# Kernel optimization log

Measured on AMD Instinct MI355X. Metric: run time of the kernel, lower is better.

Reference implementation:

```python
import jax, jax.numpy as jnp
import numpy as np

V = 50257   # vocab size (output_size / num_words)
H = 500     # hidden_size
S = 256     # source sequence length
MAXLEN = 64 # greedy decode steps
SOS = 1


def _gru_scan(xs, Wih, Whh, bih, bhh, reverse=False):
    """Run a GRU over xs: (S, Din) -> (outputs (S,H), final hidden (H,)).
    PyTorch gate order: r, z, n."""
    gx = xs @ Wih.T + bih  # (S, 3H), input-side gates precomputed
    Hh = Whh.shape[1]
    h0 = jnp.zeros((Hh,), dtype=xs.dtype)

    def step(h, g):
        gh = Whh @ h + bhh
        rx, zx, nx = jnp.split(g, 3)
        rh, zh, nh = jnp.split(gh, 3)
        r = jax.nn.sigmoid(rx + rh)
        z = jax.nn.sigmoid(zx + zh)
        n = jnp.tanh(nx + r * nh)
        h2 = (1.0 - z) * n + z * h
        return h2, h2

    hT, ys = jax.lax.scan(step, h0, gx, reverse=reverse)
    return ys, hT


def _gru_cell(x, h, Wih, Whh, bih, bhh):
    gx = Wih @ x + bih
    gh = Whh @ h + bhh
    rx, zx, nx = jnp.split(gx, 3)
    rh, zh, nh = jnp.split(gh, 3)
    r = jax.nn.sigmoid(rx + rh)
    z = jax.nn.sigmoid(zx + zh)
    n = jnp.tanh(nx + r * nh)
    return (1.0 - z) * n + z * h


def setup_inputs() -> dict:
    key = jax.random.key(0)
    ks = jax.random.split(key, 32)

    def p(k, shape):
        return jax.random.normal(k, shape, dtype=jnp.float32) * 0.05

    inp = {}
    inp["input_seq"] = jax.random.randint(ks[0], (S, 1), 0, V)
    inp["input_length"] = S
    inp["max_length"] = MAXLEN
    inp["emb"] = p(ks[1], (V, H))
    i = 2
    for name, din in [("enc0f", H), ("enc0b", H), ("enc1f", 2 * H), ("enc1b", 2 * H)]:
        inp[name + "_Wih"] = p(ks[i], (3 * H, din)); i += 1
        inp[name + "_Whh"] = p(ks[i], (3 * H, H)); i += 1
        inp[name + "_bih"] = p(ks[i], (3 * H,)); i += 1
        inp[name + "_bhh"] = p(ks[i], (3 * H,)); i += 1
    inp["dec_Wih"] = p(ks[i], (2, 3 * H, H)); i += 1
    inp["dec_Whh"] = p(ks[i], (2, 3 * H, H)); i += 1
    inp["dec_bih"] = p(ks[i], (2, 3 * H)); i += 1
    inp["dec_bhh"] = p(ks[i], (2, 3 * H)); i += 1
    inp["concat_W"] = p(ks[i], (H, 2 * H)); i += 1
    inp["concat_b"] = p(ks[i], (H,)); i += 1
    inp["out_W"] = p(ks[i], (V, H)); i += 1
    inp["out_b"] = p(ks[i], (V,)); i += 1
    return inp


def reference(input_seq, input_length, max_length, emb,
              enc0f_Wih, enc0f_Whh, enc0f_bih, enc0f_bhh,
              enc0b_Wih, enc0b_Whh, enc0b_bih, enc0b_bhh,
              enc1f_Wih, enc1f_Whh, enc1f_bih, enc1f_bhh,
              enc1b_Wih, enc1b_Whh, enc1b_bih, enc1b_bhh,
              dec_Wih, dec_Whh, dec_bih, dec_bhh,
              concat_W, concat_b, out_W, out_b):
    tokens = input_seq[:, 0]  # batch = 1
    ex = emb[tokens]          # (S, H) embedding lookup (dropout is eval no-op)

    # --- bidirectional 2-layer encoder GRU (full-length seq, batch=1) ---
    y0f, h0f = _gru_scan(ex, enc0f_Wih, enc0f_Whh, enc0f_bih, enc0f_bhh)
    y0b, h0b = _gru_scan(ex, enc0b_Wih, enc0b_Whh, enc0b_bih, enc0b_bhh, reverse=True)
    x1 = jnp.concatenate([y0f, y0b], axis=1)  # (S, 2H)
    y1f, _ = _gru_scan(x1, enc1f_Wih, enc1f_Whh, enc1f_bih, enc1f_bhh)
    y1b, _ = _gru_scan(x1, enc1b_Wih, enc1b_Whh, enc1b_bih, enc1b_bhh, reverse=True)
    enc_out = y1f + y1b  # (S, H): outputs[:, :H] + outputs[:, H:]

    # encoder_hidden[:n_layers] = [layer0_fwd, layer0_bwd] (PyTorch ordering)
    h_dec0 = jnp.stack([h0f, h0b])  # (2, H)

    def step(carry, _):
        h, tok = carry
        x = emb[tok]  # (H,)
        hs = []
        for l in range(2):  # 2 decoder GRU layers (dropout off in eval)
            hl = _gru_cell(x, h[l], dec_Wih[l], dec_Whh[l], dec_bih[l], dec_bhh[l])
            hs.append(hl)
            x = hl
        h2 = jnp.stack(hs)
        rnn = x  # (H,) top-layer output
        scores = enc_out @ rnn                 # dot attention: (S,)
        w = jax.nn.softmax(scores)
        ctx = w @ enc_out                      # (H,)
        c = jnp.tanh(concat_W @ jnp.concatenate([rnn, ctx]) + concat_b)
        probs = jax.nn.softmax(out_W @ c + out_b)  # (V,)
        tok2 = jnp.argmax(probs).astype(jnp.int32)
        return (h2, tok2), (tok2, probs)

    init = (h_dec0, jnp.asarray(SOS, dtype=jnp.int32))
    _, (all_tokens, all_probs) = jax.lax.scan(step, init, None, length=int(max_length))
    return all_tokens, all_probs
```

## Files before the change

kernel.cpp:

```cpp
#include <hip/hip_runtime.h>
#include <math.h>

typedef unsigned long long ull;

constexpr int H    = 500;
constexpr int H3   = 1500;
constexpr int SEQ  = 256;
constexpr int V    = 50257;
constexpr int TDEC = 64;
constexpr int NLT  = (V + 255) / 256;
constexpr int SB   = 50;
constexpr int UPB  = 10;
constexpr int NDB  = 512;
constexpr int VPB  = (V + NDB - 1) / NDB;
constexpr int WB   = 63;

__device__ __forceinline__ float sigmoidf_(float x) { return 1.f / (1.f + expf(-x)); }

__device__ __forceinline__ float wred(float v) {
  #pragma unroll
  for (int off = 32; off > 0; off >>= 1) v += __shfl_down(v, off, 64);
  return v;
}

__device__ __forceinline__ float gload(const float* p) {
  return __hip_atomic_load((float*)p, __ATOMIC_RELAXED, __HIP_MEMORY_SCOPE_AGENT);
}
__device__ __forceinline__ void gstore(float* p, float v) {
  __hip_atomic_store(p, v, __ATOMIC_RELAXED, __HIP_MEMORY_SCOPE_AGENT);
}
__device__ __forceinline__ int gload_i(const int* p) {
  return __hip_atomic_load((int*)p, __ATOMIC_RELAXED, __HIP_MEMORY_SCOPE_AGENT);
}
__device__ __forceinline__ ull gload64(const ull* p) {
  return __hip_atomic_load((ull*)p, __ATOMIC_RELAXED, __HIP_MEMORY_SCOPE_AGENT);
}
__device__ __forceinline__ void gstore64(ull* p, ull v) {
  __hip_atomic_store(p, v, __ATOMIC_RELAXED, __HIP_MEMORY_SCOPE_AGENT);
}

template<int N, int SLP>
__device__ __forceinline__ void poll_tags(const ull* tags, unsigned want,
                                          float* dst, int tid) {
  constexpr int NW = (N + 63) / 64;
  if (tid < 64) {
    ull v[NW];
    bool ok;
    do {
      ok = true;
      #pragma unroll
      for (int j = 0; j < NW; ++j) {
        int k = tid + (j << 6);
        if (k < N) {
          v[j] = gload64(&tags[k]);
          if ((unsigned)(v[j] >> 32) != want) ok = false;
        }
      }
      if (!ok) __builtin_amdgcn_s_sleep(SLP);
    } while (!ok);
    #pragma unroll
    for (int j = 0; j < NW; ++j) {
      int k = tid + (j << 6);
      if (k < N) dst[k] = __uint_as_float((unsigned)v[j]);
    }
  }
  __syncthreads();
}

__device__ __forceinline__ void poll2_tags(const ull* tA, float* dA,
                                           const ull* tB, float* dB,
                                           unsigned want, int tid) {
  if (tid < 64) {
    ull va[8], vb[4];
    bool ok;
    do {
      ok = true;
      #pragma unroll
      for (int j = 0; j < 8; ++j) {
        int k = tid + (j << 6);
        if (k < 500) {
          va[j] = gload64(&tA[k]);
          if ((unsigned)(va[j] >> 32) != want) ok = false;
        }
      }
      #pragma unroll
      for (int j = 0; j < 4; ++j) {
        int k = tid + (j << 6);
        vb[j] = gload64(&tB[k]);
        if ((unsigned)(vb[j] >> 32) != want) ok = false;
      }
      if (!ok) __builtin_amdgcn_s_sleep(1);
    } while (!ok);
    #pragma unroll
    for (int j = 0; j < 8; ++j) {
      int k = tid + (j << 6);
      if (k < 500) dA[k] = __uint_as_float((unsigned)va[j]);
    }
    #pragma unroll
    for (int j = 0; j < 4; ++j) {
      int k = tid + (j << 6);
      dB[k] = __uint_as_float((unsigned)vb[j]);
    }
  }
  __syncthreads();
}

__global__ void init_k(ull* ttok) {
  if (threadIdx.x == 0) ttok[0] = (1ull << 32) | 1ull;
}

__global__ void embed_k(const int* __restrict__ seq, const float* __restrict__ emb,
                        float* __restrict__ ex) {
  int t = blockIdx.x;
  int tok = seq[t];
  for (int i = threadIdx.x; i < H; i += blockDim.x)
    ex[(size_t)t * H + i] = emb[(size_t)tok * H + i];
}

__global__ __launch_bounds__(256) void gemm_nt(const float* __restrict__ X,
                                               const float* __restrict__ W,
                                               const float* __restrict__ bias,
                                               float* __restrict__ C,
                                               int M, int N, int K) {
  __shared__ float Xs[64][17];
  __shared__ float Ws[64][17];
  int bm = blockIdx.y * 64, bn = blockIdx.x * 64;
  int tid = threadIdx.x;
  int tx = tid % 16, ty = tid / 16;
  float acc[4][4] = {};
  for (int k0 = 0; k0 < K; k0 += 16) {
    for (int i = tid; i < 64 * 16; i += 256) {
      int m = i / 16, k = i % 16;
      int gm = bm + m, gk = k0 + k, gn = bn + m;
      Xs[m][k] = (gm < M && gk < K) ? X[(size_t)gm * K + gk] : 0.f;
      Ws[m][k] = (gn < N && gk < K) ? W[(size_t)gn * K + gk] : 0.f;
    }
    __syncthreads();
    #pragma unroll
    for (int k = 0; k < 16; ++k) {
      float xv[4], wv[4];
      #pragma unroll
      for (int i = 0; i < 4; ++i) xv[i] = Xs[ty * 4 + i][k];
      #pragma unroll
      for (int j = 0; j < 4; ++j) wv[j] = Ws[tx * 4 + j][k];
      #pragma unroll
      for (int i = 0; i < 4; ++i)
        #pragma unroll
        for (int j = 0; j < 4; ++j) acc[i][j] += xv[i] * wv[j];
    }
    __syncthreads();
  }
  for (int i = 0; i < 4; ++i) {
    int gm = bm + ty * 4 + i;
    if (gm >= M) continue;
    for (int j = 0; j < 4; ++j) {
      int gn = bn + tx * 4 + j;
      if (gn >= N) continue;
      C[(size_t)gm * N + gn] = acc[i][j] + bias[gn];
    }
  }
}

__global__ __launch_bounds__(512, 1) void gru_scan_tag(
    const float* __restrict__ gxF, const float* __restrict__ gxB,
    const float* __restrict__ WhhF, const float* __restrict__ WhhB,
    const float* __restrict__ bhhF, const float* __restrict__ bhhB,
    ull* __restrict__ tAF, ull* __restrict__ tBF,
    ull* __restrict__ tAB, ull* __restrict__ tBB,
    float* __restrict__ yF, float* __restrict__ yB, int ystride) {
  __shared__ float gates[32];
  __shared__ float h_lds[512];
  int dir = blockIdx.x / SB;
  int bu  = blockIdx.x % SB;
  int u0  = bu * UPB;
  const float* gx  = dir ? gxB : gxF;
  const float* Whh = dir ? WhhB : WhhF;
  const float* bhh = dir ? bhhB : bhhF;
  ull* tagA = dir ? tAB : tAF;
  ull* tagB = dir ? tBB : tBF;
  float* y  = dir ? yB : yF;
  int tid = threadIdx.x, lane = tid & 63, wid = tid >> 6;

  float wreg[4][8];
  #pragma unroll
  for (int rr = 0; rr < 4; ++rr) {
    int r = wid + 8 * rr;
    #pragma unroll
    for (int j = 0; j < 8; ++j) {
      int k = lane + 64 * j;
      wreg[rr][j] = (r < 30 && k < 500)
          ? Whh[(size_t)((r / UPB) * 500 + u0 + (r % UPB)) * 500 + k] : 0.f;
    }
  }
  int u = u0 + tid;
  float br = 0.f, bz = 0.f, bn = 0.f;
  if (tid < UPB) { br = bhh[u]; bz = bhh[500 + u]; bn = bhh[1000 + u]; }
  h_lds[tid] = 0.f;
  __syncthreads();

  for (int t = 0; t < SEQ; ++t) {
    ull* wout = (t & 1) ? tagA : tagB;
    ull* win  = (t & 1) ? tagB : tagA;
    int teff = dir ? (SEQ - 1 - t) : t;

    float gxr = 0.f, gxz = 0.f, gxn = 0.f;
    if (tid < UPB) {
      const float* g = gx + (size_t)teff * H3;
      gxr = g[u]; gxz = g[500 + u]; gxn = g[1000 + u];
    }

    if (t > 0 && wid == 0) {
      ull v[8];
      for (;;) {
        bool ok = true;
        #pragma unroll
        for (int j = 0; j < 8; ++j) {
          int k = lane + 64 * j;
          if (k < 500) {
            v[j] = gload64(&win[k]);
            if ((unsigned)(v[j] >> 32) != (unsigned)t) ok = false;
          }
        }
        if (ok) break;
        __builtin_amdgcn_s_sleep(1);
      }
      #pragma unroll
      for (int j = 0; j < 8; ++j) {
        int k = lane + 64 * j;
        if (k < 500) h_lds[k] = __uint_as_float((unsigned)v[j]);
      }
    }
    __syncthreads();

    float hold = (tid < UPB) ? h_lds[u] : 0.f;
    float hreg[8];
    #pragma unroll
    for (int j = 0; j < 8; ++j) {
      int k = lane + 64 * j;
      hreg[j] = (k < 500) ? h_lds[k] : 0.f;
    }
    #pragma unroll
    for (int rr = 0; rr < 4; ++rr) {
      int r = wid + 8 * rr;
      if (r < 30) {
        float acc = 0.f;
        #pragma unroll
        for (int j = 0; j < 8; ++j) acc += wreg[rr][j] * hreg[j];
        acc = wred(acc);
        if (lane == 0) gates[r] = acc;
      }
    }
    __syncthreads();
    if (tid < UPB) {
      float rr = sigmoidf_(gxr + gates[tid]           + br);
      float zz = sigmoidf_(gxz + gates[UPB + tid]     + bz);
      float nn = tanhf(    gxn + rr * (gates[2 * UPB + tid] + bn));
      float hp = (1.f - zz) * nn + zz * hold;
      ull pv = ((ull)(unsigned)(t + 1) << 32) | (ull)__float_as_uint(hp);
      gstore64(&wout[u], pv);
      y[(size_t)teff * ystride + u] = hp;
    }
  }
}

__global__ void seed_k(const ull* __restrict__ tf, const ull* __restrict__ tb,
                       ull* __restrict__ th0a, ull* __restrict__ th1a) {
  int i = threadIdx.x;
  if (i < 500) {
    th0a[i] = (ull)(unsigned)tf[i];
    th1a[i] = (ull)(unsigned)tb[i];
  }
}

__global__ void add_k(const float* __restrict__ a, const float* __restrict__ b,
                      float* __restrict__ c, int n) {
  int i = blockIdx.x * blockDim.x + threadIdx.x;
  if (i < n) c[i] = a[i] + b[i];
}

__global__ __launch_bounds__(256) void transposeE_k(const float* __restrict__ A,
                                                    float* __restrict__ B) {
  __shared__ float t[64][65];
  int c0 = blockIdx.x * 64;
  int r0 = blockIdx.y * 64;
  int tx = threadIdx.x & 63, ty = threadIdx.x >> 6;
  #pragma unroll
  for (int i = 0; i < 64; i += 4) {
    int r = r0 + ty + i, c = c0 + tx;
    if (r < SEQ && c < 500) t[ty + i][tx] = A[(size_t)r * 500 + c];
  }
  __syncthreads();
  #pragma unroll
  for (int i = 0; i < 64; i += 4) {
    int c = c0 + ty + i, r = r0 + tx;
    if (c < 500 && r < SEQ) B[(size_t)c * SEQ + r] = t[tx][ty + i];
  }
}

__device__ __forceinline__ void cell_unit_tag(int u, int lane,
    const float* xf, const float* hf,
    const float* __restrict__ Wih, const float* __restrict__ Whh,
    const float* __restrict__ bih, const float* __restrict__ bhh,
    ull* htag, unsigned want) {
  float g[6];
  #pragma unroll
  for (int kind = 0; kind < 6; ++kind) {
    const float* row = (kind < 3) ? (Wih + (size_t)(kind * 500 + u) * 500)
                                  : (Whh + (size_t)((kind - 3) * 500 + u) * 500);
    const float* vec = (kind < 3) ? xf : hf;
    float acc = 0.f;
    #pragma unroll
    for (int j = 0; j < 8; ++j) {
      int k = lane + 64 * j;
      if (k < 500) acc += row[k] * vec[k];
    }
    g[kind] = wred(acc);
  }
  if (lane == 0) {
    float r = sigmoidf_(g[0] + bih[u]        + g[3] + bhh[u]);
    float z = sigmoidf_(g[1] + bih[500 + u]  + g[4] + bhh[500 + u]);
    float n = tanhf(    g[2] + bih[1000 + u] + r * (g[5] + bhh[1000 + u]));
    float hv = (1.f - z) * n + z * hf[u];
    gstore64(&htag[u], ((ull)want << 32) | (ull)__float_as_uint(hv));
  }
}

__global__ __launch_bounds__(512, 4) void dec_persist(
    const float* __restrict__ emb,
    const float* __restrict__ dWih, const float* __restrict__ dWhh,
    const float* __restrict__ dbih, const float* __restrict__ dbhh,
    const float* __restrict__ enc_out, const float* __restrict__ enc_outT,
    const float* __restrict__ cW, const float* __restrict__ cb,
    const float* __restrict__ outW, const float* __restrict__ outb,
    ull* __restrict__ th0a, ull* __restrict__ th0b,
    ull* __restrict__ th1a, ull* __restrict__ th1b,
    ull* __restrict__ tsc, ull* __restrict__ tctx, ull* __restrict__ tcvec,
    ull* __restrict__ ttok,
    float* __restrict__ lg0, float* __restrict__ lg1,
    float* __restrict__ pm, float* __restrict__ ps, int* __restrict__ pix,
    float* __restrict__ stats, float* __restrict__ out_tokens,
    float* __restrict__ out_probs, int* __restrict__ dcnt) {
  __shared__ float4 v4[250];
  __shared__ float hfull[512];
  __shared__ float red[256], sc[256];
  __shared__ float wm[8], wsum[8]; __shared__ int wix[8];
  __shared__ float mm[512], ms[512]; __shared__ int mi[512];
  __shared__ int lastf, sh_tk;
  float* xf = (float*)v4;
  float* hf = xf + 500;
  int tid = threadIdx.x, lane = tid & 63, wid = tid >> 6, blk = blockIdx.x;
  bool worker = blk < WB;
  int u = blk * 8 + wid;

  for (int st = 0; st < TDEC; ++st) {
    unsigned want = (unsigned)(st + 1);
    ull* h0r = (st & 1) ? th0b : th0a;
    ull* h0w = (st & 1) ? th0a : th0b;
    ull* h1r = (st & 1) ? th1b : th1a;
    ull* h1w = (st & 1) ? th1a : th1b;
    float* lg_w = (st & 1) ? lg1 : lg0;
    const float* lg_r = (st & 1) ? lg0 : lg1;

    if (worker) {
      if (tid == 0) {
        ull tv;
        for (;;) {
          tv = gload64(ttok);
          if ((unsigned)(tv >> 32) == want) break;
          __builtin_amdgcn_s_sleep(1);
        }
        sh_tk = (int)(unsigned)tv;
      }
      __syncthreads();
      int tk = sh_tk;
      if (tid >= 64) {
        for (int i = tid - 64; i < 500; i += 448) xf[i] = emb[(size_t)tk * 500 + i];
      } else {
        #pragma unroll
        for (int j = 0; j < 8; ++j) {
          int k = tid + (j << 6);
          if (k < 500) hf[k] = __uint_as_float((unsigned)gload64(&h0r[k]));
        }
      }
      __syncthreads();
      if (u < 500) cell_unit_tag(u, lane, xf, hf, dWih, dWhh, dbih, dbhh, h0w, want);
      __syncthreads();

      if (tid >= 64) {
        for (int i = tid - 64; i < 500; i += 448)
          hf[i] = __uint_as_float((unsigned)gload64(&h1r[i]));
      }
      poll_tags<500, 1>(h0w, want, xf, tid);
      if (u < 500) cell_unit_tag(u, lane, xf, hf,
          dWih + 750000, dWhh + 750000, dbih + 1500, dbhh + 1500, h1w, want);
      __syncthreads();

      if (blk < 32) {
        poll_tags<500, 1>(h1w, want, hfull, tid);
        int s = blk * 8 + wid;
        const float* row = enc_out + (size_t)s * 500;
        float acc = 0.f;
        #pragma unroll
        for (int j = 0; j < 8; ++j) {
          int k = lane + 64 * j;
          if (k < 500) acc += row[k] * hfull[k];
        }
        acc = wred(acc);
        if (lane == 0) gstore64(&tsc[s], ((ull)want << 32) | (ull)__float_as_uint(acc));
        poll_tags<256, 1>(tsc, want, sc, tid);
      } else {
        poll2_tags(h1w, hfull, tsc, sc, want, tid);
      }

      {
        float myv = (tid < 256) ? sc[tid] : 0.f;
        if (tid < 256) red[tid] = myv;
        __syncthreads();
        for (int s = 128; s > 0; s >>= 1) {
          if (tid < s) red[tid] = fmaxf(red[tid], red[tid + s]);
          __syncthreads();
        }
        float m = red[0]; __syncthreads();
        float e = 0.f;
        if (tid < 256) { e = expf(myv - m); red[tid] = e; }
        __syncthreads();
        for (int s = 128; s > 0; s >>= 1) {
          if (tid < s) red[tid] += red[tid + s];
          __syncthreads();
        }
        float inv = 1.f / red[0]; __syncthreads();
        if (tid < 256) sc[tid] = e * inv;
        __syncthreads();
        int j = blk * 8 + wid;
        if (j < 500) {
          const float* col = enc_outT + (size_t)j * SEQ;
          float acc = 0.f;
          #pragma unroll
          for (int q = 0; q < 4; ++q) {
            int s = lane + 64 * q;
            acc += sc[s] * col[s];
          }
          acc = wred(acc);
          if (lane == 0) gstore64(&tctx[j], ((ull)want << 32) | (ull)__float_as_uint(acc));
        }
      }

      if (tid >= 64) for (int i = tid - 64; i < 500; i += 448) xf[i] = hfull[i];
      poll_tags<500, 1>(tctx, want, hf, tid);
      {
        int i = blk * 8 + wid;
        if (i < 500) {
          const float* row = cW + (size_t)i * 1000;
          float acc = 0.f;
          #pragma unroll
          for (int j = 0; j < 16; ++j) {
            int k = lane + 64 * j;
            if (k < 1000) acc += row[k] * xf[k];
          }
          acc = wred(acc);
          if (lane == 0)
            gstore64(&tcvec[i], ((ull)want << 32) | (ull)__float_as_uint(tanhf(acc + cb[i])));
        }
      }
      __syncthreads();
    } else {
      if (tid == 0) {
        while ((unsigned)(gload64(ttok) >> 32) < want) __builtin_amdgcn_s_sleep(2);
      }
      __syncthreads();
      if (st > 0) {
        float mM = gload(&stats[2 * (st - 1)]), iS = gload(&stats[2 * (st - 1) + 1]);
        int base = blk * VPB;
        for (int r = tid; r < VPB; r += 512) {
          int v = base + r;
          if (v < V) out_probs[(size_t)(st - 1) * V + v] = expf(lg_r[v] - mM) * iS;
        }
      }
    }

    if (worker) poll_tags<500, 1>(tcvec, want, xf, tid);
    else        poll_tags<500, 4>(tcvec, want, xf, tid);
    const float4* c4 = v4;
    {
      int lstart = wid * 13, lend = lstart + 13;
      if (lstart > VPB) lstart = VPB;
      if (lend > VPB) lend = VPB;
      int r0 = blk * VPB + lstart, r1 = blk * VPB + lend; if (r1 > V) r1 = V;
      float m = -1e30f, ssum = 0.f; int ix = V;
      for (int rb = r0; rb < r1; rb += 8) {
        int nr = r1 - rb; if (nr > 8) nr = 8;
        float4 wv0[8], wv1[8];
        #pragma unroll
        for (int rr = 0; rr < 8; ++rr) {
          wv0[rr] = (lane < 125 && rr < nr)
              ? ((const float4*)(outW + (size_t)(rb + rr) * 500))[lane]
              : make_float4(0.f, 0.f, 0.f, 0.f);
        }
        #pragma unroll
        for (int rr = 0; rr < 8; ++rr) {
          int k4 = lane + 64;
          wv1[rr] = (k4 < 125 && rr < nr)
              ? ((const float4*)(outW + (size_t)(rb + rr) * 500))[k4]
              : make_float4(0.f, 0.f, 0.f, 0.f);
        }
        float a[8];
        #pragma unroll
        for (int rr = 0; rr < 8; ++rr) a[rr] = 0.f;
        if (lane < 125) {
          float4 cc = c4[lane];
          #pragma unroll
          for (int rr = 0; rr < 8; ++rr) {
            if (rr < nr) {
              float4 w4 = wv0[rr];
              a[rr] += w4.x * cc.x + w4.y * cc.y + w4.z * cc.z + w4.w * cc.w;
            }
          }
        }
        if (lane + 64 < 125) {
          float4 cc = c4[lane + 64];
          #pragma unroll
          for (int rr = 0; rr < 8; ++rr) {
            if (rr < nr) {
              float4 w4 = wv1[rr];
              a[rr] += w4.x * cc.x + w4.y * cc.y + w4.z * cc.z + w4.w * cc.w;
            }
          }
        }
        #pragma unroll
        for (int rr = 0; rr < 8; ++rr) {
          if (rr < nr) {
            float l = wred(a[rr]);
            if (lane == 0) {
              l += outb[rb + rr];
              lg_w[rb + rr] = l;
              if (l > m) { ssum = ssum * expf(m - l) + 1.f; m = l; ix = rb + rr; }
              else       { ssum += expf(l - m); }
            }
          }
        }
      }
      if (lane == 0) { wm[wid] = m; wsum[wid] = ssum; wix[wid] = ix; }
    }
    __syncthreads();
    if (tid == 0) {
      float M = wm[0], S = wsum[0]; int I = wix[0];
      for (int w2 = 1; w2 < 8; ++w2) {
        if (wm[w2] > M) { S = S * expf(M - wm[w2]) + wsum[w2]; M = wm[w2]; I = wix[w2]; }
        else            { S += wsum[w2] * expf(wm[w2] - M); }
      }
      gstore(&pm[blk], M); gstore(&ps[blk], S);
      __hip_atomic_store(&pix[blk], I, __ATOMIC_RELAXED, __HIP_MEMORY_SCOPE_AGENT);
      __builtin_amdgcn_s_waitcnt(0);
      int prev = __hip_atomic_fetch_add(&dcnt[st], 1, __ATOMIC_RELAXED,
                                        __HIP_MEMORY_SCOPE_AGENT);
      lastf = (prev == NDB - 1) ? 1 : 0;
    }
    __syncthreads();

    if (lastf) {
      { mm[tid] = gload(&pm[tid]); ms[tid] = gload(&ps[tid]); mi[tid] = gload_i(&pix[tid]); }
      __syncthreads();
      for (int s = 256; s > 0; s >>= 1) {
        if (tid < s) {
          float ma = mm[tid], mb = mm[tid + s];
          float sa = ms[tid], sb = ms[tid + s];
          int ia = mi[tid], ib = mi[tid + s];
          if (mb > ma || (mb == ma && ib < ia)) {
            ms[tid] = sa * expf(ma - mb) + sb; mm[tid] = mb; mi[tid] = ib;
          } else {
            ms[tid] = sa + sb * expf(mb - ma);
          }
        }
        __syncthreads();
      }
      if (tid == 0) {
        out_tokens[st] = (float)mi[0];
        gstore(&stats[2 * st], mm[0]);
        gstore(&stats[2 * st + 1], 1.f / ms[0]);
        __builtin_amdgcn_s_waitcnt(0);
        gstore64(ttok, ((ull)(unsigned)(st + 2) << 32) | (ull)(unsigned)mi[0]);
      }
    }

    if (worker && st > 0) {
      float mM = gload(&stats[2 * (st - 1)]), iS = gload(&stats[2 * (st - 1) + 1]);
      int base = blk * VPB;
      for (int r = tid; r < VPB; r += 512) {
        int v = base + r;
        if (v < V) out_probs[(size_t)(st - 1) * V + v] = expf(lg_r[v] - mM) * iS;
      }
    }
    __syncthreads();
  }
}

__global__ __launch_bounds__(256) void probs_k(const float* __restrict__ logits,
    const float* __restrict__ stats, float* __restrict__ out_probs) {
  int v = blockIdx.x * 256 + threadIdx.x;
  if (v < V) out_probs[v] = expf(logits[v] - stats[0]) * stats[1];
}

extern "C" void kernel_launch(void* const* d_in, const int* in_sizes, int n_in,
                              void* d_out, int out_size, void* d_ws, size_t ws_size,
                              hipStream_t stream) {
  const int*   seq   = (const int*)d_in[0];
  const float* emb   = (const float*)d_in[3];
  const float* e0f_Wih = (const float*)d_in[4];
  const float* e0f_Whh = (const float*)d_in[5];
  const float* e0f_bih = (const float*)d_in[6];
  const float* e0f_bhh = (const float*)d_in[7];
  const float* e0b_Wih = (const float*)d_in[8];
  const float* e0b_Whh = (const float*)d_in[9];
  const float* e0b_bih = (const float*)d_in[10];
  const float* e0b_bhh = (const float*)d_in[11];
  const float* e1f_Wih = (const float*)d_in[12];
  const float* e1f_Whh = (const float*)d_in[13];
  const float* e1f_bih = (const float*)d_in[14];
  const float* e1f_bhh = (const float*)d_in[15];
  const float* e1b_Wih = (const float*)d_in[16];
  const float* e1b_Whh = (const float*)d_in[17];
  const float* e1b_bih = (const float*)d_in[18];
  const float* e1b_bhh = (const float*)d_in[19];
  const float* dWih = (const float*)d_in[20];
  const float* dWhh = (const float*)d_in[21];
  const float* dbih = (const float*)d_in[22];
  const float* dbhh = (const float*)d_in[23];
  const float* cW   = (const float*)d_in[24];
  const float* cb   = (const float*)d_in[25];
  const float* outW = (const float*)d_in[26];
  const float* outb = (const float*)d_in[27];

  float* w = (float*)d_ws;
  float* ex      = w;
  float* x1      = ex + 128000;
  float* gxf     = x1 + 256000;
  float* gxb     = gxf + 384000;
  float* y1f     = gxb + 384000;
  float* y1b     = y1f + 128000;
  float* enc_out = y1b + 128000;
  float* lg0     = enc_out + 128000;
  float* lg1     = lg0 + 50432;
  float* pm      = lg1 + 50432;
  float* ps      = pm + 512;
  float* stats   = ps + 512;
  int*   pix     = (int*)(stats + 192);
  int*   dcnt    = pix + 512;
  ull*   htag    = (ull*)(dcnt + 64);
  ull* tL0F_A = htag;        ull* tL0F_B = htag + 512;
  ull* tL0B_A = htag + 1024; ull* tL0B_B = htag + 1536;
  ull* tL1F_A = htag + 2048; ull* tL1F_B = htag + 2560;
  ull* tL1B_A = htag + 3072; ull* tL1B_B = htag + 3584;
  ull*   dtag    = htag + 4096;
  ull* th0a  = dtag;        ull* th0b = dtag + 512;
  ull* th1a  = dtag + 1024; ull* th1b = dtag + 1536;
  ull* tsc   = dtag + 2048; ull* tctx = dtag + 2304;
  ull* tcvec = dtag + 2816; ull* ttok = dtag + 3328;
  float* enc_outT = (float*)(dtag + 3400);

  float* outf = (float*)d_out;

  (void)hipMemsetAsync(dcnt, 0, 64 * sizeof(int) + 7488 * sizeof(ull), stream);

  init_k<<<1, 64, 0, stream>>>(ttok);
  embed_k<<<SEQ, 128, 0, stream>>>(seq, emb, ex);

  gemm_nt<<<dim3(24, 4), 256, 0, stream>>>(ex, e0f_Wih, e0f_bih, gxf, SEQ, H3, H);
  gemm_nt<<<dim3(24, 4), 256, 0, stream>>>(ex, e0b_Wih, e0b_bih, gxb, SEQ, H3, H);
  gru_scan_tag<<<2 * SB, 512, 0, stream>>>(gxf, gxb, e0f_Whh, e0b_Whh,
      e0f_bhh, e0b_bhh, tL0F_A, tL0F_B, tL0B_A, tL0B_B, x1, x1 + 500, 1000);

  gemm_nt<<<dim3(24, 4), 256, 0, stream>>>(x1, e1f_Wih, e1f_bih, gxf, SEQ, H3, 2 * H);
  gemm_nt<<<dim3(24, 4), 256, 0, stream>>>(x1, e1b_Wih, e1b_bih, gxb, SEQ, H3, 2 * H);
  gru_scan_tag<<<2 * SB, 512, 0, stream>>>(gxf, gxb, e1f_Whh, e1b_Whh,
      e1f_bhh, e1b_bhh, tL1F_A, tL1F_B, tL1B_A, tL1B_B, y1f, y1b, 500);
  add_k<<<(SEQ * H + 255) / 256, 256, 0, stream>>>(y1f, y1b, enc_out, SEQ * H);
  transposeE_k<<<dim3(8, 4), 256, 0, stream>>>(enc_out, enc_outT);

  seed_k<<<1, 512, 0, stream>>>(tL0F_A, tL0B_A, th0a, th1a);

  dec_persist<<<NDB, 512, 0, stream>>>(emb,
      dWih, dWhh, dbih, dbhh, enc_out, enc_outT, cW, cb, outW, outb,
      th0a, th0b, th1a, th1b, tsc, tctx, tcvec, ttok,
      lg0, lg1, pm, ps, pix, stats, outf, outf + TDEC, dcnt);

  probs_k<<<NLT, 256, 0, stream>>>(((TDEC - 1) & 1) ? lg1 : lg0,
      stats + 2 * (TDEC - 1), outf + TDEC + (size_t)(TDEC - 1) * V);
}
```

Measured before the change: 6.786 ms.

## Keep output-projection rows resident in registers and replace atomic counter reduction with tagged slots

Non-worker blocks of the persistent decoder now load their share of out_W (12 rows per wave) into registers once before the decode loop and reuse them on every step, while worker blocks handle the leftover rows by streaming them from memory. This is meant to remove the repeated ~100MB out_W read from global memory on each of the 64 steps. The per-step global softmax reduction drops the atomic last-block counter: each block publishes a tagged max/sum/index, and block 0 polls for all of them. This adds register pressure (24 float4 per thread) that may cut occupancy or cause spills, and it puts the final reduction on a single block.

```diff
diff --git a/kernel.cpp b/kernel.cpp
--- a/kernel.cpp
+++ b/kernel.cpp
@@ -12,8 +12,11 @@
 constexpr int SB   = 50;
 constexpr int UPB  = 10;
 constexpr int NDB  = 512;
-constexpr int VPB  = (V + NDB - 1) / NDB;
-constexpr int WB   = 63;
+constexpr int WKB  = 63;
+constexpr int RPW  = 12;
+constexpr int NWR  = 8 * RPW;
+constexpr int RREG = (NDB - WKB) * NWR;
+constexpr int WSR  = (V - RREG + WKB - 1) / WKB;
 
 __device__ __forceinline__ float sigmoidf_(float x) { return 1.f / (1.f + expf(-x)); }
 
@@ -28,9 +31,6 @@
 }
 __device__ __forceinline__ void gstore(float* p, float v) {
   __hip_atomic_store(p, v, __ATOMIC_RELAXED, __HIP_MEMORY_SCOPE_AGENT);
-}
-__device__ __forceinline__ int gload_i(const int* p) {
-  return __hip_atomic_load((int*)p, __ATOMIC_RELAXED, __HIP_MEMORY_SCOPE_AGENT);
 }
 __device__ __forceinline__ ull gload64(const ull* p) {
   return __hip_atomic_load((ull*)p, __ATOMIC_RELAXED, __HIP_MEMORY_SCOPE_AGENT);
@@ -335,22 +335,36 @@
     ull* __restrict__ th0a, ull* __restrict__ th0b,
     ull* __restrict__ th1a, ull* __restrict__ th1b,
     ull* __restrict__ tsc, ull* __restrict__ tctx, ull* __restrict__ tcvec,
-    ull* __restrict__ ttok,
+    ull* __restrict__ ttok, ull* __restrict__ pmt, ull* __restrict__ psix,
     float* __restrict__ lg0, float* __restrict__ lg1,
-    float* __restrict__ pm, float* __restrict__ ps, int* __restrict__ pix,
     float* __restrict__ stats, float* __restrict__ out_tokens,
-    float* __restrict__ out_probs, int* __restrict__ dcnt) {
+    float* __restrict__ out_probs) {
   __shared__ float4 v4[250];
   __shared__ float hfull[512];
   __shared__ float red[256], sc[256];
   __shared__ float wm[8], wsum[8]; __shared__ int wix[8];
   __shared__ float mm[512], ms[512]; __shared__ int mi[512];
-  __shared__ int lastf, sh_tk;
+  __shared__ int sh_tk;
   float* xf = (float*)v4;
   float* hf = xf + 500;
   int tid = threadIdx.x, lane = tid & 63, wid = tid >> 6, blk = blockIdx.x;
-  bool worker = blk < WB;
+  bool worker = blk < WKB;
   int u = blk * 8 + wid;
+
+  float4 wa[RPW], wb[RPW];
+  int regbase = 0;
+  if (!worker) {
+    regbase = (blk - WKB) * NWR + wid * RPW;
+    const float4* w4 = (const float4*)outW;
+    #pragma unroll
+    for (int rr = 0; rr < RPW; ++rr) {
+      size_t ro = (size_t)(regbase + rr) * 125;
+      wa[rr] = (lane < 125) ? w4[ro + lane] : make_float4(0.f, 0.f, 0.f, 0.f);
+      wb[rr] = (lane + 64 < 125) ? w4[ro + lane + 64] : make_float4(0.f, 0.f, 0.f, 0.f);
+    }
+  }
+  int srow0 = RREG + blk * WSR;
+  int snr   = V - srow0; if (snr > WSR) snr = WSR; if (snr < 0) snr = 0;
 
   for (int st = 0; st < TDEC; ++st) {
     unsigned want = (unsigned)(st + 1);
@@ -470,71 +484,92 @@
       __syncthreads();
       if (st > 0) {
         float mM = gload(&stats[2 * (st - 1)]), iS = gload(&stats[2 * (st - 1) + 1]);
-        int base = blk * VPB;
-        for (int r = tid; r < VPB; r += 512) {
+        int base = (blk - WKB) * NWR;
+        for (int r = tid; r < NWR; r += 512) {
           int v = base + r;
-          if (v < V) out_probs[(size_t)(st - 1) * V + v] = expf(lg_r[v] - mM) * iS;
+          out_probs[(size_t)(st - 1) * V + v] = expf(lg_r[v] - mM) * iS;
         }
       }
     }
 
     if (worker) poll_tags<500, 1>(tcvec, want, xf, tid);
-    else        poll_tags<500, 4>(tcvec, want, xf, tid);
+    else        poll_tags<500, 16>(tcvec, want, xf, tid);
     const float4* c4 = v4;
     {
-      int lstart = wid * 13, lend = lstart + 13;
-      if (lstart > VPB) lstart = VPB;
-      if (lend > VPB) lend = VPB;
-      int r0 = blk * VPB + lstart, r1 = blk * VPB + lend; if (r1 > V) r1 = V;
       float m = -1e30f, ssum = 0.f; int ix = V;
-      for (int rb = r0; rb < r1; rb += 8) {
-        int nr = r1 - rb; if (nr > 8) nr = 8;
-        float4 wv0[8], wv1[8];
+      if (!worker) {
+        float4 cc0 = (lane < 125) ? c4[lane] : make_float4(0.f, 0.f, 0.f, 0.f);
+        float4 cc1 = (lane + 64 < 125) ? c4[lane + 64] : make_float4(0.f, 0.f, 0.f, 0.f);
         #pragma unroll
-        for (int rr = 0; rr < 8; ++rr) {
-          wv0[rr] = (lane < 125 && rr < nr)
-              ? ((const float4*)(outW + (size_t)(rb + rr) * 500))[lane]
-              : make_float4(0.f, 0.f, 0.f, 0.f);
-        }
-        #pragma unroll
-        for (int rr = 0; rr < 8; ++rr) {
-          int k4 = lane + 64;
-          wv1[rr] = (k4 < 125 && rr < nr)
-              ? ((const float4*)(outW + (size_t)(rb + rr) * 500))[k4]
-              : make_float4(0.f, 0.f, 0.f, 0.f);
-        }
-        float a[8];
-        #pragma unroll
-        for (int rr = 0; rr < 8; ++rr) a[rr] = 0.f;
-        if (lane < 125) {
-          float4 cc = c4[lane];
+        for (int rr = 0; rr < RPW; ++rr) {
+          float a = 0.f;
+          if (lane < 125)
+            a += wa[rr].x * cc0.x + wa[rr].y * cc0.y + wa[rr].z * cc0.z + wa[rr].w * cc0.w;
+          if (lane + 64 < 125)
+            a += wb[rr].x * cc1.x + wb[rr].y * cc1.y + wb[rr].z * cc1.z + wb[rr].w * cc1.w;
+          float l = wred(a);
+          if (lane == 0) {
+            int row = regbase + rr;
+            l += outb[row];
+            lg_w[row] = l;
+            if (l > m) { ssum = ssum * expf(m - l) + 1.f; m = l; ix = row; }
+            else       { ssum += expf(l - m); }
+          }
+        }
+      } else {
+        int ls = wid * 15, le = ls + 15;
+        if (ls > snr) ls = snr;
+        if (le > snr) le = snr;
+        int r0 = srow0 + ls, r1 = srow0 + le;
+        for (int rb = r0; rb < r1; rb += 8) {
+          int nr = r1 - rb; if (nr > 8) nr = 8;
+          float4 wv0[8], wv1[8];
+          #pragma unroll
+          for (int rr = 0; rr < 8; ++rr) {
+            wv0[rr] = (lane < 125 && rr < nr)
+                ? ((const float4*)(outW + (size_t)(rb + rr) * 500))[lane]
+                : make_float4(0.f, 0.f, 0.f, 0.f);
+          }
+          #pragma unroll
+          for (int rr = 0; rr < 8; ++rr) {
+            int k4 = lane + 64;
+            wv1[rr] = (k4 < 125 && rr < nr)
+                ? ((const float4*)(outW + (size_t)(rb + rr) * 500))[k4]
+                : make_float4(0.f, 0.f, 0.f, 0.f);
+          }
+          float a[8];
+          #pragma unroll
+          for (int rr = 0; rr < 8; ++rr) a[rr] = 0.f;
+          if (lane < 125) {
+            float4 cc = c4[lane];
+            #pragma unroll
+            for (int rr = 0; rr < 8; ++rr) {
+              if (rr < nr) {
+                float4 w4 = wv0[rr];
+                a[rr] += w4.x * cc.x + w4.y * cc.y + w4.z * cc.z + w4.w * cc.w;
+              }
+            }
+          }
+          if (lane + 64 < 125) {
+            float4 cc = c4[lane + 64];
+            #pragma unroll
+            for (int rr = 0; rr < 8; ++rr) {
+              if (rr < nr) {
+                float4 w4 = wv1[rr];
+                a[rr] += w4.x * cc.x + w4.y * cc.y + w4.z * cc.z + w4.w * cc.w;
+              }
+            }
+          }
           #pragma unroll
           for (int rr = 0; rr < 8; ++rr) {
             if (rr < nr) {
-              float4 w4 = wv0[rr];
-              a[rr] += w4.x * cc.x + w4.y * cc.y + w4.z * cc.z + w4.w * cc.w;
-            }
-          }
-        }
-        if (lane + 64 < 125) {
-          float4 cc = c4[lane + 64];
-          #pragma unroll
-          for (int rr = 0; rr < 8; ++rr) {
-            if (rr < nr) {
-              float4 w4 = wv1[rr];
-              a[rr] += w4.x * cc.x + w4.y * cc.y + w4.z * cc.z + w4.w * cc.w;
-            }
-          }
-        }
-        #pragma unroll
-        for (int rr = 0; rr < 8; ++rr) {
-          if (rr < nr) {
-            float l = wred(a[rr]);
-            if (lane == 0) {
-              l += outb[rb + rr];
-              lg_w[rb + rr] = l;
-              if (l > m) { ssum = ssum * expf(m - l) + 1.f; m = l; ix = rb + rr; }
-              else       { ssum += expf(l - m); }
+              float l = wred(a[rr]);
+              if (lane == 0) {
+                l += outb[rb + rr];
+                lg_w[rb + rr] = l;
+                if (l > m) { ssum = ssum * expf(m - l) + 1.f; m = l; ix = rb + rr; }
+                else       { ssum += expf(l - m); }
+              }
             }
           }
         }
@@ -548,17 +583,22 @@
         if (wm[w2] > M) { S = S * expf(M - wm[w2]) + wsum[w2]; M = wm[w2]; I = wix[w2]; }
         else            { S += wsum[w2] * expf(wm[w2] - M); }
       }
-      gstore(&pm[blk], M); gstore(&ps[blk], S);
-      __hip_atomic_store(&pix[blk], I, __ATOMIC_RELAXED, __HIP_MEMORY_SCOPE_AGENT);
+      gstore64(&psix[blk], ((ull)__float_as_uint(S) << 32) | (ull)(unsigned)I);
       __builtin_amdgcn_s_waitcnt(0);
-      int prev = __hip_atomic_fetch_add(&dcnt[st], 1, __ATOMIC_RELAXED,
-                                        __HIP_MEMORY_SCOPE_AGENT);
-      lastf = (prev == NDB - 1) ? 1 : 0;
+      gstore64(&pmt[blk], ((ull)want << 32) | (ull)__float_as_uint(M));
     }
     __syncthreads();
 
-    if (lastf) {
-      { mm[tid] = gload(&pm[tid]); ms[tid] = gload(&ps[tid]); mi[tid] = gload_i(&pix[tid]); }
+    if (blk == 0) {
+      {
+        ull tv;
+        while ((unsigned)((tv = gload64(&pmt[tid])) >> 32) != want)
+          __builtin_amdgcn_s_sleep(2);
+        mm[tid] = __uint_as_float((unsigned)tv);
+        ull sv = gload64(&psix[tid]);
+        ms[tid] = __uint_as_float((unsigned)(sv >> 32));
+        mi[tid] = (int)(unsigned)sv;
+      }
       __syncthreads();
       for (int s = 256; s > 0; s >>= 1) {
         if (tid < s) {
@@ -580,14 +620,14 @@
         __builtin_amdgcn_s_waitcnt(0);
         gstore64(ttok, ((ull)(unsigned)(st + 2) << 32) | (ull)(unsigned)mi[0]);
       }
+      __syncthreads();
     }
 
     if (worker && st > 0) {
       float mM = gload(&stats[2 * (st - 1)]), iS = gload(&stats[2 * (st - 1) + 1]);
-      int base = blk * VPB;
-      for (int r = tid; r < VPB; r += 512) {
-        int v = base + r;
-        if (v < V) out_probs[(size_t)(st - 1) * V + v] = expf(lg_r[v] - mM) * iS;
+      for (int r = tid; r < snr; r += 512) {
+        int v = srow0 + r;
+        out_probs[(size_t)(st - 1) * V + v] = expf(lg_r[v] - mM) * iS;
       }
     }
     __syncthreads();
@@ -640,12 +680,8 @@
   float* enc_out = y1b + 128000;
   float* lg0     = enc_out + 128000;
   float* lg1     = lg0 + 50432;
-  float* pm      = lg1 + 50432;
-  float* ps      = pm + 512;
-  float* stats   = ps + 512;
-  int*   pix     = (int*)(stats + 192);
-  int*   dcnt    = pix + 512;
-  ull*   htag    = (ull*)(dcnt + 64);
+  float* stats   = lg1 + 50432;
+  ull*   htag    = (ull*)(stats + 192);
   ull* tL0F_A = htag;        ull* tL0F_B = htag + 512;
   ull* tL0B_A = htag + 1024; ull* tL0B_B = htag + 1536;
   ull* tL1F_A = htag + 2048; ull* tL1F_B = htag + 2560;
@@ -655,11 +691,12 @@
   ull* th1a  = dtag + 1024; ull* th1b = dtag + 1536;
   ull* tsc   = dtag + 2048; ull* tctx = dtag + 2304;
   ull* tcvec = dtag + 2816; ull* ttok = dtag + 3328;
-  float* enc_outT = (float*)(dtag + 3400);
+  ull* pmt   = dtag + 3392; ull* psix = dtag + 3904;
+  float* enc_outT = (float*)(dtag + 4416);
 
   float* outf = (float*)d_out;
 
-  (void)hipMemsetAsync(dcnt, 0, 64 * sizeof(int) + 7488 * sizeof(ull), stream);
+  (void)hipMemsetAsync(htag, 0, (4096 + 4416) * sizeof(ull), stream);
 
   init_k<<<1, 64, 0, stream>>>(ttok);
   embed_k<<<SEQ, 128, 0, stream>>>(seq, emb, ex);
@@ -680,8 +717,8 @@
 
   dec_persist<<<NDB, 512, 0, stream>>>(emb,
       dWih, dWhh, dbih, dbhh, enc_out, enc_outT, cW, cb, outW, outb,
-      th0a, th0b, th1a, th1b, tsc, tctx, tcvec, ttok,
-      lg0, lg1, pm, ps, pix, stats, outf, outf + TDEC, dcnt);
+      th0a, th0b, th1a, th1b, tsc, tctx, tcvec, ttok, pmt, psix,
+      lg0, lg1, stats, outf, outf + TDEC);
 
   probs_k<<<NLT, 256, 0, stream>>>(((TDEC - 1) & 1) ? lg1 : lg0,
       stats + 2 * (TDEC - 1), outf + TDEC + (size_t)(TDEC - 1) * V);
```

Measured after the change: 7.249 ms. 6.8% more time.
